# Kernel optimization log

Hardware: AMD Instinct MI355X
Metric: run time of the kernel (lower is better)

## Reference

```python
import jax, jax.numpy as jnp
import numpy as np

N, D, C, S = 100000, 512, 4096, 50000


def setup_inputs() -> dict:
    key = jax.random.key(0)
    k1, k2 = jax.random.split(key)
    X = jax.random.normal(k1, (N, D), dtype=jnp.float32)
    codebook_sum = jax.random.normal(k2, (C, D), dtype=jnp.float32)
    prompt_mask = jnp.arange(N) < S  # first S rows are support (True), rest are queries
    return {"X": X, "codebook_sum": codebook_sum, "prompt_mask": prompt_mask, "num_support": S}


def reference(X, codebook_sum, prompt_mask, num_support):
    # num_support is a static Python int (replaces torch.nonzero(prompt_mask) dynamic split)
    s = num_support
    support = X[:s]                                   # [S, D] support (prompt_mask==True)
    query = X[s:]                                     # [Q, D] queries (prompt_mask==False)
    # dense similarity matmul + top-1 nearest-codebook search + gather
    cos_sim = jnp.einsum('sd,cd->sc', support, codebook_sum)  # [S, C]
    top_idx = jnp.argmax(cos_sim, axis=1)             # [S]
    code_n = codebook_sum[top_idx]                    # [S, D] gathered nearest codes
    # mean-pooled prototypes broadcast over queries
    proto = jnp.mean(support, axis=0)                 # [D]
    proto_code = jnp.mean(code_n, axis=0)             # [D]
    # euclidean distances to each prototype
    query_score = jnp.sqrt(jnp.sum((query - proto) ** 2, axis=1))        # [Q]
    query_score_code = jnp.sqrt(jnp.sum((query - proto_code) ** 2, axis=1))  # [Q]
    return (query_score + query_score_code) / 2
```

## Files before the change

kernel.cpp:

```cpp
#include <hip/hip_runtime.h>
#include <hip/hip_bf16.h>

#define NTOT 100000
#define DIM  512
#define CB   4096
#define SSUP 50000
#define NQ   (NTOT - SSUP)

#define MTILES 391
#define MPAD   (MTILES * 128)
#define NTILES 32

typedef __bf16 bf16x8 __attribute__((ext_vector_type(8)));
typedef __bf16 bf16x4 __attribute__((ext_vector_type(4)));
typedef float  f32x4  __attribute__((ext_vector_type(4)));

#define OFF_CBBF   0
#define OFF_XB     4194304
#define OFF_PV     55443456
#define OFF_PI     61849600
#define OFF_PSUM   68255744
#define OFF_PCSUM  68257792
#define OFF_HIST   68259840
#define WS_NEED    (68259840 + 16384)
#define ZERO_BYTES (2048 + 2048 + 16384)

#define F_OFF_PSUM   4194304
#define F_OFF_PCSUM  4196352
#define F_OFF_HIST   4198400
#define F_OFF_TIDX   4214784

__device__ __forceinline__ void load_lds16(const void* g, void* l) {
    __builtin_amdgcn_global_load_lds(
        (const __attribute__((address_space(1))) void*)g,
        (__attribute__((address_space(3))) void*)l, 16, 0, 0);
}

__global__ void k_convert(const float* __restrict__ src, __bf16* __restrict__ dst) {
    int i = (blockIdx.x * 256 + threadIdx.x) * 4;
    float4 v = *(const float4*)(src + i);
    bf16x4 o;
    o[0] = (__bf16)v.x; o[1] = (__bf16)v.y; o[2] = (__bf16)v.z; o[3] = (__bf16)v.w;
    *(bf16x4*)(dst + i) = o;
}

__global__ void k_prep_support(const float* __restrict__ X, __bf16* __restrict__ Xb,
                               float* __restrict__ protoSum) {
    const int tid   = threadIdx.x;
    const int rhalf = tid >> 7;
    const int c4    = (tid & 127) * 4;
    const size_t r0 = (size_t)blockIdx.x * 128;
    float a0 = 0.f, a1 = 0.f, a2 = 0.f, a3 = 0.f;
    for (int i = 0; i < 64; ++i) {
        size_t r = r0 + (size_t)i * 2 + rhalf;
        float4 v = *(const float4*)(X + r * DIM + c4);
        bf16x4 o;
        o[0] = (__bf16)v.x; o[1] = (__bf16)v.y; o[2] = (__bf16)v.z; o[3] = (__bf16)v.w;
        *(bf16x4*)(Xb + r * DIM + c4) = o;
        if (r < SSUP) { a0 += v.x; a1 += v.y; a2 += v.z; a3 += v.w; }
    }
    atomicAdd(&protoSum[c4 + 0], a0);
    atomicAdd(&protoSum[c4 + 1], a1);
    atomicAdd(&protoSum[c4 + 2], a2);
    atomicAdd(&protoSum[c4 + 3], a3);
}

__global__ __launch_bounds__(256)
void k_gemm_tile(const __bf16* __restrict__ Xb, const __bf16* __restrict__ cbb,
                 float* __restrict__ pv, int* __restrict__ pi)
{
    __shared__ __bf16 lA[128 * 32];
    __shared__ __bf16 lB[128 * 32];
    __shared__ float  sv[128][2];
    __shared__ int    si[128][2];

    const int tid  = threadIdx.x;
    const int wave = tid >> 6;
    const int lane = tid & 63;
    const int wm   = wave >> 1;
    const int wn   = wave & 1;
    const int l15  = lane & 15;
    const int q    = lane >> 4;
    const int nt   = blockIdx.x;
    const int mt   = blockIdx.y;
    const size_t r0 = (size_t)mt * 128;
    const int    c0 = nt * 128;

    f32x4 acc[4][4];
    #pragma unroll
    for (int i = 0; i < 4; ++i)
        #pragma unroll
        for (int j = 0; j < 4; ++j)
            acc[i][j] = (f32x4){0.f, 0.f, 0.f, 0.f};

    for (int k0 = 0; k0 < 512; k0 += 32) {
        __syncthreads();
        #pragma unroll
        for (int i = 0; i < 2; ++i) {
            const int ck  = i * 256 + tid;
            const int row = ck >> 2;
            const int kc  = ck & 3;
            load_lds16(Xb  + (r0 + row) * DIM + k0 + kc * 8, lA + ck * 8);
            load_lds16(cbb + (size_t)(c0 + row) * DIM + k0 + kc * 8, lB + ck * 8);
        }
        __syncthreads();

        bf16x8 af[4], bfr[4];
        #pragma unroll
        for (int t = 0; t < 4; ++t) {
            af[t]  = *(const bf16x8*)(lA + (wm * 64 + t * 16 + l15) * 32 + q * 8);
            bfr[t] = *(const bf16x8*)(lB + (wn * 64 + t * 16 + l15) * 32 + q * 8);
        }
        #pragma unroll
        for (int tm = 0; tm < 4; ++tm)
            #pragma unroll
            for (int tn = 0; tn < 4; ++tn)
                acc[tm][tn] = __builtin_amdgcn_mfma_f32_16x16x32_bf16(
                    af[tm], bfr[tn], acc[tm][tn], 0, 0, 0);
    }

    #pragma unroll
    for (int tm = 0; tm < 4; ++tm) {
        #pragma unroll
        for (int reg = 0; reg < 4; ++reg) {
            float v = -3.0e38f; int idx = 0;
            #pragma unroll
            for (int tn = 0; tn < 4; ++tn) {
                float x = acc[tm][tn][reg];
                int   c = c0 + wn * 64 + tn * 16 + l15;
                if (x > v) { v = x; idx = c; }
            }
            #pragma unroll
            for (int off = 1; off < 16; off <<= 1) {
                float ov = __shfl_xor(v, off, 64);
                int   oi = __shfl_xor(idx, off, 64);
                if (ov > v) { v = ov; idx = oi; }
            }
            if (l15 == 0) {
                int rl = wm * 64 + tm * 16 + q * 4 + reg;
                sv[rl][wn] = v;
                si[rl][wn] = idx;
            }
        }
    }
    __syncthreads();
    if (tid < 128) {
        float v0 = sv[tid][0], v1 = sv[tid][1];
        pv[(size_t)nt * MPAD + r0 + tid] = fmaxf(v0, v1);
        pi[(size_t)nt * MPAD + r0 + tid] = (v1 > v0) ? si[tid][1] : si[tid][0];
    }
}

__global__ void k_reduce_hist(const float* __restrict__ pv, const int* __restrict__ pi,
                              int* __restrict__ hist) {
    __shared__ int lh[CB];
    for (int i = threadIdx.x; i < CB; i += 256) lh[i] = 0;
    __syncthreads();
    int r = blockIdx.x * 256 + threadIdx.x;
    if (r < SSUP) {
        float v = -3.0e38f; int idx = 0;
        #pragma unroll 8
        for (int j = 0; j < 32; ++j) {
            float x = pv[(size_t)j * MPAD + r];
            if (x > v) { v = x; idx = pi[(size_t)j * MPAD + r]; }
        }
        atomicAdd(&lh[idx], 1);
    }
    __syncthreads();
    for (int i = threadIdx.x; i < CB; i += 256) {
        int v = lh[i];
        if (v) atomicAdd(&hist[i], v);
    }
}

__global__ void k_proto_code(const float* __restrict__ cb, const int* __restrict__ hist,
                             float* __restrict__ pcSum) {
    const int d  = threadIdx.x;
    const int c0 = blockIdx.x * 64;
    float acc = 0.f;
    for (int c = c0; c < c0 + 64; ++c) {
        float w = (float)hist[c];
        if (w != 0.f) acc += w * cb[(size_t)c * DIM + d];
    }
    atomicAdd(&pcSum[d], acc);
}

__global__ void k_query(const float* __restrict__ X, const float* __restrict__ protoSum,
                        const float* __restrict__ pcSum, float* __restrict__ out) {
    const int lane   = threadIdx.x & 63;
    const int waveId = (blockIdx.x * blockDim.x + threadIdx.x) >> 6;
    const int nwaves = (gridDim.x * blockDim.x) >> 6;
    const float invS = 1.0f / (float)SSUP;

    for (int r = waveId; r < NQ; r += nwaves) {
        const float* xr = X + (size_t)(SSUP + r) * DIM;
        float s1 = 0.f, s2 = 0.f;
        #pragma unroll
        for (int i = 0; i < 2; ++i) {
            int dd = lane * 4 + i * 256;
            float4 xq = *(const float4*)(xr + dd);
            float4 p  = *(const float4*)(protoSum + dd);
            float4 pc = *(const float4*)(pcSum + dd);
            float d0, d1, d2, d3;
            d0 = xq.x - p.x * invS; d1 = xq.y - p.y * invS;
            d2 = xq.z - p.z * invS; d3 = xq.w - p.w * invS;
            s1 += d0 * d0 + d1 * d1 + d2 * d2 + d3 * d3;
            d0 = xq.x - pc.x * invS; d1 = xq.y - pc.y * invS;
            d2 = xq.z - pc.z * invS; d3 = xq.w - pc.w * invS;
            s2 += d0 * d0 + d1 * d1 + d2 * d2 + d3 * d3;
        }
        #pragma unroll
        for (int off = 32; off > 0; off >>= 1) {
            s1 += __shfl_xor(s1, off, 64);
            s2 += __shfl_xor(s2, off, 64);
        }
        if (lane == 0)
            out[r] = 0.5f * (sqrtf(s1) + sqrtf(s2));
    }
}

__global__ __launch_bounds__(256, 2)
void k_gemm_argmax(const float* __restrict__ X, const __bf16* __restrict__ cbb,
                   int* __restrict__ top_idx)
{
    __shared__ float redv[64][2];
    __shared__ int   redi[64][2];

    const int tid  = threadIdx.x;
    const int wave = tid >> 6;
    const int lane = tid & 63;
    const int wm   = wave >> 1;
    const int wn   = wave & 1;
    const int l15  = lane & 15;
    const int q    = lane >> 4;
    const int r0   = blockIdx.x * 64;

    bf16x8 aflat[2][16];
    #pragma unroll
    for (int tm = 0; tm < 2; ++tm) {
        const int r = r0 + wm * 32 + tm * 16 + l15;
        const bool valid = (r < SSUP);
        const float* xr = X + (size_t)r * DIM + q * 8;
        #pragma unroll
        for (int kt = 0; kt < 16; ++kt) {
            float4 v0, v1;
            if (valid) {
                v0 = *(const float4*)(xr + kt * 32);
                v1 = *(const float4*)(xr + kt * 32 + 4);
            } else {
                v0 = make_float4(0.f, 0.f, 0.f, 0.f);
                v1 = v0;
            }
            bf16x8 f;
            f[0] = (__bf16)v0.x; f[1] = (__bf16)v0.y; f[2] = (__bf16)v0.z; f[3] = (__bf16)v0.w;
            f[4] = (__bf16)v1.x; f[5] = (__bf16)v1.y; f[6] = (__bf16)v1.z; f[7] = (__bf16)v1.w;
            aflat[tm][kt] = f;
        }
    }

    float mx[8]; int mi[8];
    #pragma unroll
    for (int i = 0; i < 8; ++i) { mx[i] = -3.0e38f; mi[i] = 0; }
    const f32x4 zero4 = {0.f, 0.f, 0.f, 0.f};

    for (int ct = 0; ct < 32; ++ct) {
        const int c0 = ct * 128 + wn * 64;
        const __bf16* bptr[4];
        #pragma unroll
        for (int tn = 0; tn < 4; ++tn)
            bptr[tn] = cbb + (size_t)(c0 + tn * 16 + l15) * DIM + q * 8;

        f32x4 acc[2][4];
        #pragma unroll
        for (int i = 0; i < 2; ++i)
            #pragma unroll
            for (int j = 0; j < 4; ++j)
                acc[i][j] = zero4;

        #pragma unroll
        for (int kt = 0; kt < 16; ++kt) {
            bf16x8 b[4];
            #pragma unroll
            for (int tn = 0; tn < 4; ++tn)
                b[tn] = *(const bf16x8*)(bptr[tn] + kt * 32);
            #pragma unroll
            for (int tm = 0; tm < 2; ++tm)
                #pragma unroll
                for (int tn = 0; tn < 4; ++tn)
                    acc[tm][tn] = __builtin_amdgcn_mfma_f32_16x16x32_bf16(
                        aflat[tm][kt], b[tn], acc[tm][tn], 0, 0, 0);
        }
        #pragma unroll
        for (int tm = 0; tm < 2; ++tm)
            #pragma unroll
            for (int tn = 0; tn < 4; ++tn)
                #pragma unroll
                for (int reg = 0; reg < 4; ++reg) {
                    float v = acc[tm][tn][reg];
                    int slot = tm * 4 + reg;
                    int col  = c0 + tn * 16 + l15;
                    if (v > mx[slot]) { mx[slot] = v; mi[slot] = col; }
                }
    }

    #pragma unroll
    for (int slot = 0; slot < 8; ++slot) {
        float v  = mx[slot];
        int  idx = mi[slot];
        #pragma unroll
        for (int off = 1; off < 16; off <<= 1) {
            float ov = __shfl_xor(v, off, 64);
            int   oi = __shfl_xor(idx, off, 64);
            if (ov > v) { v = ov; idx = oi; }
        }
        if (l15 == 0) {
            int rowl = wm * 32 + (slot >> 2) * 16 + q * 4 + (slot & 3);
            redv[rowl][wn] = v;
            redi[rowl][wn] = idx;
        }
    }
    __syncthreads();
    if (tid < 64) {
        int r = r0 + tid;
        if (r < SSUP) {
            float v0 = redv[tid][0], v1 = redv[tid][1];
            top_idx[r] = (v1 > v0) ? redi[tid][1] : redi[tid][0];
        }
    }
}

__global__ void k_proto_sum(const float* __restrict__ X, float* __restrict__ protoSum) {
    const int d = threadIdx.x;
    const int r0 = blockIdx.x * 500;
    float acc = 0.f;
    for (int r = r0; r < r0 + 500; ++r)
        acc += X[(size_t)r * DIM + d];
    atomicAdd(&protoSum[d], acc);
}

__global__ void k_hist(const int* __restrict__ top_idx, int* __restrict__ hist) {
    __shared__ int lh[CB];
    for (int i = threadIdx.x; i < CB; i += blockDim.x) lh[i] = 0;
    __syncthreads();
    for (int i = blockIdx.x * blockDim.x + threadIdx.x; i < SSUP; i += gridDim.x * blockDim.x)
        atomicAdd(&lh[top_idx[i]], 1);
    __syncthreads();
    for (int i = threadIdx.x; i < CB; i += blockDim.x) {
        int v = lh[i];
        if (v) atomicAdd(&hist[i], v);
    }
}

extern "C" void kernel_launch(void* const* d_in, const int* in_sizes, int n_in,
                              void* d_out, int out_size, void* d_ws, size_t ws_size,
                              hipStream_t stream) {
    const float* X  = (const float*)d_in[0];
    const float* cb = (const float*)d_in[1];
    float* out = (float*)d_out;
    char* ws = (char*)d_ws;

    __bf16* cbb = (__bf16*)(ws + OFF_CBBF);

    if (ws_size >= (size_t)WS_NEED) {
        __bf16* Xb       = (__bf16*)(ws + OFF_XB);
        float*  pv       = (float*)(ws + OFF_PV);
        int*    pi       = (int*)(ws + OFF_PI);
        float*  protoSum = (float*)(ws + OFF_PSUM);
        float*  pcSum    = (float*)(ws + OFF_PCSUM);
        int*    hist     = (int*)(ws + OFF_HIST);

        hipMemsetAsync(ws + OFF_PSUM, 0, ZERO_BYTES, stream);

        k_convert<<<(CB * DIM) / 1024, 256, 0, stream>>>(cb, cbb);
        k_prep_support<<<MTILES, 256, 0, stream>>>(X, Xb, protoSum);

        dim3 grid(NTILES, MTILES);
        k_gemm_tile<<<grid, 256, 0, stream>>>(Xb, cbb, pv, pi);

        k_reduce_hist<<<(SSUP + 255) / 256, 256, 0, stream>>>(pv, pi, hist);
        k_proto_code<<<CB / 64, 512, 0, stream>>>(cb, hist, pcSum);
        k_query<<<1024, 256, 0, stream>>>(X, protoSum, pcSum, out);
    } else {
        float*  protoSum = (float*)(ws + F_OFF_PSUM);
        float*  pcSum    = (float*)(ws + F_OFF_PCSUM);
        int*    hist     = (int*)(ws + F_OFF_HIST);
        int*    top_idx  = (int*)(ws + F_OFF_TIDX);

        hipMemsetAsync(ws + F_OFF_PSUM, 0, ZERO_BYTES, stream);

        k_convert<<<(CB * DIM) / 1024, 256, 0, stream>>>(cb, cbb);
        k_proto_sum<<<100, 512, 0, stream>>>(X, protoSum);
        k_gemm_argmax<<<(SSUP + 63) / 64, 256, 0, stream>>>(X, cbb, top_idx);
        k_hist<<<64, 256, 0, stream>>>(top_idx, hist);
        k_proto_code<<<CB / 64, 512, 0, stream>>>(cb, hist, pcSum);
        k_query<<<1024, 256, 0, stream>>>(X, protoSum, pcSum, out);
    }
}
```

Before: 666.3 us.

## Switch GEMM to 32x32 MFMA with swizzled LDS and XCD-aware tile mapping

The main GEMM kernel now uses 32x32x16 bf16 MFMA instructions in place of 16x16x32. It XOR-swizzles the LDS layout to avoid bank conflicts on fragment reads, and remaps the 1D block index so that blocks sharing an M tile land on the same XCD for L2 reuse. Several smaller knobs also change: an unroll pragma in the support prep, more blocks for proto_code and the query kernel, and a variable rename. The argmax epilogue is rewritten for the 32x32 accumulator layout, which risks index mapping errors.

```diff
diff --git a/kernel.cpp b/kernel.cpp
--- a/kernel.cpp
+++ b/kernel.cpp
@@ -10,10 +10,12 @@
 #define MTILES 391
 #define MPAD   (MTILES * 128)
 #define NTILES 32
+#define NBLOCKS (MTILES * NTILES)
 
 typedef __bf16 bf16x8 __attribute__((ext_vector_type(8)));
 typedef __bf16 bf16x4 __attribute__((ext_vector_type(4)));
 typedef float  f32x4  __attribute__((ext_vector_type(4)));
+typedef float  f32x16 __attribute__((ext_vector_type(16)));
 
 #define OFF_CBBF   0
 #define OFF_XB     4194304
@@ -51,6 +53,7 @@
     const int c4    = (tid & 127) * 4;
     const size_t r0 = (size_t)blockIdx.x * 128;
     float a0 = 0.f, a1 = 0.f, a2 = 0.f, a3 = 0.f;
+    #pragma unroll 4
     for (int i = 0; i < 64; ++i) {
         size_t r = r0 + (size_t)i * 2 + rhalf;
         float4 v = *(const float4*)(X + r * DIM + c4);
@@ -79,67 +82,84 @@
     const int lane = tid & 63;
     const int wm   = wave >> 1;
     const int wn   = wave & 1;
-    const int l15  = lane & 15;
-    const int q    = lane >> 4;
-    const int nt   = blockIdx.x;
-    const int mt   = blockIdx.y;
+    const int l31  = lane & 31;
+    const int lh   = lane >> 5;
+
+    const int b = blockIdx.x;
+    int mt, nt;
+    if (b < 12288) {
+        const int xcd = b & 7, q = b >> 3;
+        nt = q & 31;
+        mt = ((q >> 5) << 3) + xcd;
+    } else {
+        const int idx = b - 12288;
+        mt = 384 + (idx >> 5);
+        nt = idx & 31;
+    }
     const size_t r0 = (size_t)mt * 128;
     const int    c0 = nt * 128;
 
-    f32x4 acc[4][4];
+    f32x16 acc[2][2];
     #pragma unroll
-    for (int i = 0; i < 4; ++i)
-        #pragma unroll
-        for (int j = 0; j < 4; ++j)
-            acc[i][j] = (f32x4){0.f, 0.f, 0.f, 0.f};
+    for (int i = 0; i < 2; ++i)
+        #pragma unroll
+        for (int j = 0; j < 2; ++j)
+            acc[i][j] = (f32x16)(0.f);
 
     for (int k0 = 0; k0 < 512; k0 += 32) {
         __syncthreads();
         #pragma unroll
         for (int i = 0; i < 2; ++i) {
-            const int ck  = i * 256 + tid;
-            const int row = ck >> 2;
-            const int kc  = ck & 3;
-            load_lds16(Xb  + (r0 + row) * DIM + k0 + kc * 8, lA + ck * 8);
-            load_lds16(cbb + (size_t)(c0 + row) * DIM + k0 + kc * 8, lB + ck * 8);
+            const int s   = i * 256 + tid;
+            const int row = s >> 2;
+            const int kc  = (s & 3) ^ ((row >> 1) & 3);
+            load_lds16(Xb  + (r0 + row) * DIM + k0 + kc * 8, lA + s * 8);
+            load_lds16(cbb + (size_t)(c0 + row) * DIM + k0 + kc * 8, lB + s * 8);
         }
         __syncthreads();
 
-        bf16x8 af[4], bfr[4];
-        #pragma unroll
-        for (int t = 0; t < 4; ++t) {
-            af[t]  = *(const bf16x8*)(lA + (wm * 64 + t * 16 + l15) * 32 + q * 8);
-            bfr[t] = *(const bf16x8*)(lB + (wn * 64 + t * 16 + l15) * 32 + q * 8);
-        }
-        #pragma unroll
-        for (int tm = 0; tm < 4; ++tm)
-            #pragma unroll
-            for (int tn = 0; tn < 4; ++tn)
-                acc[tm][tn] = __builtin_amdgcn_mfma_f32_16x16x32_bf16(
-                    af[tm], bfr[tn], acc[tm][tn], 0, 0, 0);
+        bf16x8 af[2][2], bf[2][2];
+        #pragma unroll
+        for (int h = 0; h < 2; ++h) {
+            const int kc = h * 2 + lh;
+            #pragma unroll
+            for (int t = 0; t < 2; ++t) {
+                const int rowA  = wm * 64 + t * 32 + l31;
+                const int slotA = rowA * 4 + (kc ^ ((rowA >> 1) & 3));
+                af[h][t] = *(const bf16x8*)(lA + slotA * 8);
+                const int rowB  = wn * 64 + t * 32 + l31;
+                const int slotB = rowB * 4 + (kc ^ ((rowB >> 1) & 3));
+                bf[h][t] = *(const bf16x8*)(lB + slotB * 8);
+            }
+        }
+        #pragma unroll
+        for (int h = 0; h < 2; ++h)
+            #pragma unroll
+            for (int tm = 0; tm < 2; ++tm)
+                #pragma unroll
+                for (int tn = 0; tn < 2; ++tn)
+                    acc[tm][tn] = __builtin_amdgcn_mfma_f32_32x32x16_bf16(
+                        af[h][tm], bf[h][tn], acc[tm][tn], 0, 0, 0);
     }
 
     #pragma unroll
-    for (int tm = 0; tm < 4; ++tm) {
-        #pragma unroll
-        for (int reg = 0; reg < 4; ++reg) {
-            float v = -3.0e38f; int idx = 0;
-            #pragma unroll
-            for (int tn = 0; tn < 4; ++tn) {
-                float x = acc[tm][tn][reg];
-                int   c = c0 + wn * 64 + tn * 16 + l15;
-                if (x > v) { v = x; idx = c; }
-            }
-            #pragma unroll
-            for (int off = 1; off < 16; off <<= 1) {
+    for (int tm = 0; tm < 2; ++tm) {
+        #pragma unroll
+        for (int reg = 0; reg < 16; ++reg) {
+            float x0 = acc[tm][0][reg], x1 = acc[tm][1][reg];
+            const int cbase = c0 + wn * 64 + l31;
+            float v; int idx;
+            if (x1 > x0) { v = x1; idx = cbase + 32; } else { v = x0; idx = cbase; }
+            #pragma unroll
+            for (int off = 1; off <= 16; off <<= 1) {
                 float ov = __shfl_xor(v, off, 64);
                 int   oi = __shfl_xor(idx, off, 64);
                 if (ov > v) { v = ov; idx = oi; }
             }
-            if (l15 == 0) {
-                int rl = wm * 64 + tm * 16 + q * 4 + reg;
-                sv[rl][wn] = v;
-                si[rl][wn] = idx;
+            if (l31 == 0) {
+                const int rowL = wm * 64 + tm * 32 + 4 * lh + (reg & 3) + 8 * (reg >> 2);
+                sv[rowL][wn] = v;
+                si[rowL][wn] = idx;
             }
         }
     }
@@ -176,9 +196,9 @@
 __global__ void k_proto_code(const float* __restrict__ cb, const int* __restrict__ hist,
                              float* __restrict__ pcSum) {
     const int d  = threadIdx.x;
-    const int c0 = blockIdx.x * 64;
+    const int c0 = blockIdx.x * 32;
     float acc = 0.f;
-    for (int c = c0; c < c0 + 64; ++c) {
+    for (int c = c0; c < c0 + 32; ++c) {
         float w = (float)hist[c];
         if (w != 0.f) acc += w * cb[(size_t)c * DIM + d];
     }
@@ -279,16 +299,16 @@
 
         #pragma unroll
         for (int kt = 0; kt < 16; ++kt) {
-            bf16x8 b[4];
+            bf16x8 bfr[4];
             #pragma unroll
             for (int tn = 0; tn < 4; ++tn)
-                b[tn] = *(const bf16x8*)(bptr[tn] + kt * 32);
+                bfr[tn] = *(const bf16x8*)(bptr[tn] + kt * 32);
             #pragma unroll
             for (int tm = 0; tm < 2; ++tm)
                 #pragma unroll
                 for (int tn = 0; tn < 4; ++tn)
                     acc[tm][tn] = __builtin_amdgcn_mfma_f32_16x16x32_bf16(
-                        aflat[tm][kt], b[tn], acc[tm][tn], 0, 0, 0);
+                        aflat[tm][kt], bfr[tn], acc[tm][tn], 0, 0, 0);
         }
         #pragma unroll
         for (int tm = 0; tm < 2; ++tm)
@@ -374,12 +394,11 @@
         k_convert<<<(CB * DIM) / 1024, 256, 0, stream>>>(cb, cbb);
         k_prep_support<<<MTILES, 256, 0, stream>>>(X, Xb, protoSum);
 
-        dim3 grid(NTILES, MTILES);
-        k_gemm_tile<<<grid, 256, 0, stream>>>(Xb, cbb, pv, pi);
+        k_gemm_tile<<<NBLOCKS, 256, 0, stream>>>(Xb, cbb, pv, pi);
 
         k_reduce_hist<<<(SSUP + 255) / 256, 256, 0, stream>>>(pv, pi, hist);
-        k_proto_code<<<CB / 64, 512, 0, stream>>>(cb, hist, pcSum);
-        k_query<<<1024, 256, 0, stream>>>(X, protoSum, pcSum, out);
+        k_proto_code<<<CB / 32, 512, 0, stream>>>(cb, hist, pcSum);
+        k_query<<<2048, 256, 0, stream>>>(X, protoSum, pcSum, out);
     } else {
         float*  protoSum = (float*)(ws + F_OFF_PSUM);
         float*  pcSum    = (float*)(ws + F_OFF_PCSUM);
```

Measured after the change: 733.9 us. +10.1%, slower.
